# Kernel tuning notes

Measured on AMD Instinct MI355X. Metric: run time of the kernel, lower is better.

## Reference

```python
import jax, jax.numpy as jnp
import numpy as np

B, T, D, A = 4, 4096, 1024, 64
RINGS = 2

def _build_graph_matrix(A, rings):
    # W[a_dst, a_src] = 1/len(neigh) for src in {a_dst-rings..a_dst+rings} within bounds (mean reduce)
    W = np.zeros((A, A), dtype=np.float32)
    for a in range(A):
        neigh = [n for n in range(a - rings, a + rings + 1) if 0 <= n < A]
        W[a, neigh] = 1.0 / len(neigh)
    return jnp.asarray(W)

def setup_inputs() -> dict:
    key = jax.random.key(0)
    k0, k1, k2 = jax.random.split(key, 3)
    x = jax.random.normal(k0, (B, T, D), dtype=jnp.float32)
    # contiguous-ish 1D region assignment of tokens to anchors
    assign = jnp.sort(jax.random.randint(k1, (T,), 0, A)).astype(jnp.int32)
    counts = jnp.clip(jnp.zeros((A,), jnp.float32).at[assign].add(1.0), 1.0, None)
    W_proj = jax.random.normal(k2, (D, D), dtype=jnp.float32) * (1.0 / np.sqrt(D))
    gate = jnp.float32(0.1)
    W_graph = _build_graph_matrix(A, RINGS)
    return {"x": x, "W_proj": W_proj, "gate": gate, "assign": assign,
            "W_graph": W_graph, "counts": counts, "hops": 1}

def reference(x, W_proj, gate, assign, W_graph, counts, hops):
    Bx, Tx, Dx = x.shape
    Ax = counts.shape[0]
    # pool_per_anchor (mean): scatter-add tokens into anchors, divide by counts
    anchor = jnp.zeros((Bx, Ax, Dx), x.dtype).at[:, assign, :].add(x)
    anchor = anchor / counts[None, :, None]
    # neighbor_aggregate: out = einsum('bcd,ac->bad', out, W) per hop
    agg = anchor
    for _ in range(max(1, int(hops))):
        agg = jnp.einsum('ac,bcd->bad', W_graph, agg)
    # broadcast_from_anchor: gather each token's anchor feature
    fb = agg[:, assign, :]  # [B,T,D]
    # residual with gated linear projection (dropout identity in eval)
    return x + (fb @ W_proj.T) * jnp.tanh(gate)
```

## Files before the change

kernel.cpp:

```cpp
#include <hip/hip_runtime.h>
#include <cmath>


typedef __attribute__((ext_vector_type(8))) short bf16x8;
typedef __attribute__((ext_vector_type(4))) float f32x4;

#define OROWS 8

__device__ inline short f2bf(float f) {
    unsigned u = __float_as_uint(f);
    return (short)((u + 0x7FFFu + ((u >> 16) & 1u)) >> 16);
}
__device__ inline int lbound(const int* __restrict__ a, int n, int v) {
    int lo = 0, hi = n;
    while (lo < hi) { int m = (lo + hi) >> 1; if (a[m] < v) lo = m + 1; else hi = m; }
    return lo;
}

__global__ __launch_bounds__(256) void prepanchor_kernel(
        const float* __restrict__ x, const float* __restrict__ counts,
        const int* __restrict__ assign, const float* __restrict__ Wg,
        const int* __restrict__ hops, const float* __restrict__ Wp,
        short* __restrict__ anchorb, short* __restrict__ Wpb, float* __restrict__ M,
        int T, int D, int A, int R) {
    __shared__ float s0[4096];
    __shared__ float s1[4096];
    int bid = blockIdx.x, tid = threadIdx.x;
    int rs = D >> 2;
    if (bid < 2 * R) {
        int u = bid >> 1, half = bid & 1;
        int b = u / A, a = u - (u / A) * A;
        int* sT = (int*)s1;
        if (tid < 2) sT[tid] = lbound(assign, T, a + tid);
        __syncthreads();
        int t0 = sT[0], t1 = sT[1];
        float inv = 1.0f / counts[a];
        int d4 = half * (rs >> 1) + (tid & 127);
        int tp = tid >> 7;
        const float4* x4 = (const float4*)x + (size_t)b * T * rs;
        float4 acc = make_float4(0.f, 0.f, 0.f, 0.f);
        int t = t0 + tp;
        const float4* p = x4 + (size_t)t * rs + d4;
        for (; t + 14 < t1; t += 16) {
            float4 v0 = p[0];
            float4 v1 = p[(size_t)2 * rs];
            float4 v2 = p[(size_t)4 * rs];
            float4 v3 = p[(size_t)6 * rs];
            float4 v4 = p[(size_t)8 * rs];
            float4 v5 = p[(size_t)10 * rs];
            float4 v6 = p[(size_t)12 * rs];
            float4 v7 = p[(size_t)14 * rs];
            acc.x += ((v0.x + v1.x) + (v2.x + v3.x)) + ((v4.x + v5.x) + (v6.x + v7.x));
            acc.y += ((v0.y + v1.y) + (v2.y + v3.y)) + ((v4.y + v5.y) + (v6.y + v7.y));
            acc.z += ((v0.z + v1.z) + (v2.z + v3.z)) + ((v4.z + v5.z) + (v6.z + v7.z));
            acc.w += ((v0.w + v1.w) + (v2.w + v3.w)) + ((v4.w + v5.w) + (v6.w + v7.w));
            p += (size_t)16 * rs;
        }
        for (; t < t1; t += 2) {
            float4 v = *p;
            acc.x += v.x; acc.y += v.y; acc.z += v.z; acc.w += v.w;
            p += (size_t)2 * rs;
        }
        float4* sA = (float4*)s0;
        sA[tid] = acc;
        __syncthreads();
        if (tid < 128) {
            float4 o = sA[tid];
            float4 q = sA[tid + 128];
            o.x = (o.x + q.x) * inv; o.y = (o.y + q.y) * inv;
            o.z = (o.z + q.z) * inv; o.w = (o.w + q.w) * inv;
            short4 ob;
            ob.x = f2bf(o.x); ob.y = f2bf(o.y); ob.z = f2bf(o.z); ob.w = f2bf(o.w);
            ((short4*)anchorb)[(size_t)u * rs + d4] = ob;
        }
    } else if (bid < 2 * R + 256) {
        long long n8 = (long long)D * D / 8;
        for (long long i = (long long)(bid - 2 * R) * 256 + tid; i < n8; i += 256LL * 256LL) {
            const float4* p = (const float4*)Wp + i * 2;
            float4 v0 = p[0], v1 = p[1];
            short4* q = (short4*)Wpb + i * 2;
            short4 o0, o1;
            o0.x = f2bf(v0.x); o0.y = f2bf(v0.y); o0.z = f2bf(v0.z); o0.w = f2bf(v0.w);
            o1.x = f2bf(v1.x); o1.y = f2bf(v1.y); o1.z = f2bf(v1.z); o1.w = f2bf(v1.w);
            q[0] = o0; q[1] = o1;
        }
    } else {
        int n = A * A;
        for (int i = tid; i < n; i += 256) s0[i] = Wg[i];
        int h = hops[0]; if (h < 1) h = 1;
        for (int it = 1; it < h; ++it) {
            __syncthreads();
            for (int i = tid; i < n; i += 256) {
                int r = i / A, c = i - (i / A) * A;
                float s = 0.f;
                for (int k = 0; k < A; ++k) s += Wg[r * A + k] * s0[k * A + c];
                s1[i] = s;
            }
            __syncthreads();
            for (int i = tid; i < n; i += 256) s0[i] = s1[i];
        }
        __syncthreads();
        for (int i = tid; i < n; i += 256) M[i] = s0[i];
    }
}

__global__ __launch_bounds__(256) void ymix_kernel(
        const short* __restrict__ anchorb, const short* __restrict__ Wpb,
        const float* __restrict__ M, float* __restrict__ Y, int D, int A) {
    __shared__ float Z_lds[64][68];
    int b = blockIdx.x, dblk = blockIdx.y;
    int tid = threadIdx.x;
    int wave = tid >> 6, lane = tid & 63;
    int rc = lane & 15, kq = lane >> 4;
    int cpair = wave >> 1, dpair = wave & 1;

    {
        const short* aB0 = anchorb + (size_t)(b * A + cpair * 32 + rc) * D + kq * 8;
        const short* aB1 = aB0 + (size_t)16 * D;
        const short* bB0 = Wpb + (size_t)(dblk * 64 + dpair * 32 + rc) * D + kq * 8;
        const short* bB1 = bB0 + (size_t)16 * D;
        f32x4 acc00 = {0.f,0.f,0.f,0.f}, acc01 = {0.f,0.f,0.f,0.f};
        f32x4 acc10 = {0.f,0.f,0.f,0.f}, acc11 = {0.f,0.f,0.f,0.f};
        for (int k = 0; k < D; k += 32) {
            bf16x8 a0 = *(const bf16x8*)(aB0 + k);
            bf16x8 a1 = *(const bf16x8*)(aB1 + k);
            bf16x8 b0 = *(const bf16x8*)(bB0 + k);
            bf16x8 b1 = *(const bf16x8*)(bB1 + k);
            acc00 = __builtin_amdgcn_mfma_f32_16x16x32_bf16(a0, b0, acc00, 0, 0, 0);
            acc01 = __builtin_amdgcn_mfma_f32_16x16x32_bf16(a0, b1, acc01, 0, 0, 0);
            acc10 = __builtin_amdgcn_mfma_f32_16x16x32_bf16(a1, b0, acc10, 0, 0, 0);
            acc11 = __builtin_amdgcn_mfma_f32_16x16x32_bf16(a1, b1, acc11, 0, 0, 0);
        }
        int zr = cpair * 32 + kq * 4;
        int zc = dpair * 32 + rc;
        #pragma unroll
        for (int j = 0; j < 4; ++j) {
            Z_lds[zr + j][zc]           = acc00[j];
            Z_lds[zr + j][zc + 16]      = acc01[j];
            Z_lds[zr + 16 + j][zc]      = acc10[j];
            Z_lds[zr + 16 + j][zc + 16] = acc11[j];
        }
    }
    __syncthreads();

    for (int i = tid; i < A * 16; i += 256) {
        int a_ = i >> 4, d4 = i & 15;
        const float* Mrow = M + (size_t)a_ * A;
        f32x4 acc = {0.f, 0.f, 0.f, 0.f};
        for (int c = 0; c < 64; ++c) {
            float w = Mrow[c];
            f32x4 z = *(const f32x4*)&Z_lds[c][d4 * 4];
            acc[0] += w * z[0]; acc[1] += w * z[1];
            acc[2] += w * z[2]; acc[3] += w * z[3];
        }
        *(f32x4*)&Y[((size_t)b * A + a_) * D + dblk * 64 + d4 * 4] = acc;
    }
}

__global__ __launch_bounds__(256) void out_kernel(
        const float* __restrict__ x, const float* __restrict__ Y,
        const int* __restrict__ assign, const float* __restrict__ gate,
        float* __restrict__ out, int T, int D, int A) {
    float tg = tanhf(gate[0]);
    int rs = D >> 2;
    int bt0 = blockIdx.x * OROWS;
    const float4* x4 = (const float4*)x;
    const float4* y4 = (const float4*)Y;
    float4* o4 = (float4*)out;
    #pragma unroll
    for (int r = 0; r < OROWS; ++r) {
        int bt = bt0 + r;
        int b = bt / T;
        int t = bt - b * T;
        int a = assign[t];
        const float4* yr = y4 + ((size_t)b * A + a) * rs;
        for (int d4 = threadIdx.x; d4 < rs; d4 += 256) {
            float4 xv = x4[(size_t)bt * rs + d4];
            float4 yv = yr[d4];
            o4[(size_t)bt * rs + d4] = make_float4(xv.x + tg * yv.x, xv.y + tg * yv.y,
                                                   xv.z + tg * yv.z, xv.w + tg * yv.w);
        }
    }
}

extern "C" void kernel_launch(void* const* d_in, const int* in_sizes, int n_in,
                              void* d_out, int out_size, void* d_ws, size_t ws_size,
                              hipStream_t stream) {
    const float* x      = (const float*)d_in[0];
    const float* Wp     = (const float*)d_in[1];
    const float* gate   = (const float*)d_in[2];
    const int*   assign = (const int*)d_in[3];
    const float* Wg     = (const float*)d_in[4];
    const float* counts = (const float*)d_in[5];
    const int*   hops   = (const int*)d_in[6];
    float* out = (float*)d_out;

    int T = in_sizes[3];
    int A = in_sizes[5];
    int D = (int)(sqrt((double)in_sizes[1]) + 0.5);
    int B = (int)(in_sizes[0] / ((long long)T * D));
    int R = B * A;

    float* M       = (float*)d_ws;
    float* Y       = M + (size_t)A * A;
    short* anchorb = (short*)(Y + (size_t)R * D);
    short* Wpb     = anchorb + (size_t)R * D;

    prepanchor_kernel<<<2 * R + 257, 256, 0, stream>>>(x, counts, assign, Wg, hops, Wp,
                                                       anchorb, Wpb, M, T, D, A, R);
    dim3 g(B, D / 64);
    ymix_kernel<<<g, 256, 0, stream>>>(anchorb, Wpb, M, Y, D, A);
    out_kernel<<<B * T / OROWS, 256, 0, stream>>>(x, Y, assign, gate, out, T, D, A);
}
```

Measured before the change: 64.69 us.

## Split anchor pooling into token partials summed inside the MFMA projection

The anchor pooling now splits each anchor's token range into four partial sums written as separate bf16 rows. The ymix GEMM folds the partials in by looping over them along K. The 1/count scaling moves into the graph mixing matrix. This raises pooling-stage parallelism, from 512 to 1024 blocks with a full row each, and drops the LDS reduction, but quadruples the GEMM K work and partial storage. Each partial is also rounded to bf16 separately, which adds rounding error.

Measured after the change: 118.0 us. 1.82x slower.

```diff
diff --git a/kernel.cpp b/kernel.cpp
--- a/kernel.cpp
+++ b/kernel.cpp
@@ -5,6 +5,7 @@
 typedef __attribute__((ext_vector_type(8))) short bf16x8;
 typedef __attribute__((ext_vector_type(4))) float f32x4;
 
+#define SP 4
 #define OROWS 8
 
 __device__ inline short f2bf(float f) {
@@ -17,65 +18,62 @@
     return lo;
 }
 
-__global__ __launch_bounds__(256) void prepanchor_kernel(
+__global__ __launch_bounds__(256) void prep_kernel(
         const float* __restrict__ x, const float* __restrict__ counts,
         const int* __restrict__ assign, const float* __restrict__ Wg,
         const int* __restrict__ hops, const float* __restrict__ Wp,
-        short* __restrict__ anchorb, short* __restrict__ Wpb, float* __restrict__ M,
+        short* __restrict__ partb, short* __restrict__ Wpb, float* __restrict__ Mp,
         int T, int D, int A, int R) {
     __shared__ float s0[4096];
     __shared__ float s1[4096];
     int bid = blockIdx.x, tid = threadIdx.x;
     int rs = D >> 2;
-    if (bid < 2 * R) {
-        int u = bid >> 1, half = bid & 1;
+    int nAB = SP * R;
+    if (bid < nAB) {
+        int part = bid & (SP - 1);
+        int u = bid >> 2;
         int b = u / A, a = u - (u / A) * A;
         int* sT = (int*)s1;
         if (tid < 2) sT[tid] = lbound(assign, T, a + tid);
         __syncthreads();
         int t0 = sT[0], t1 = sT[1];
-        float inv = 1.0f / counts[a];
-        int d4 = half * (rs >> 1) + (tid & 127);
-        int tp = tid >> 7;
+        int len = t1 - t0;
+        int p0 = t0 + (len * part) / SP;
+        int p1 = t0 + (len * (part + 1)) / SP;
         const float4* x4 = (const float4*)x + (size_t)b * T * rs;
-        float4 acc = make_float4(0.f, 0.f, 0.f, 0.f);
-        int t = t0 + tp;
-        const float4* p = x4 + (size_t)t * rs + d4;
-        for (; t + 14 < t1; t += 16) {
-            float4 v0 = p[0];
-            float4 v1 = p[(size_t)2 * rs];
-            float4 v2 = p[(size_t)4 * rs];
-            float4 v3 = p[(size_t)6 * rs];
-            float4 v4 = p[(size_t)8 * rs];
-            float4 v5 = p[(size_t)10 * rs];
-            float4 v6 = p[(size_t)12 * rs];
-            float4 v7 = p[(size_t)14 * rs];
-            acc.x += ((v0.x + v1.x) + (v2.x + v3.x)) + ((v4.x + v5.x) + (v6.x + v7.x));
-            acc.y += ((v0.y + v1.y) + (v2.y + v3.y)) + ((v4.y + v5.y) + (v6.y + v7.y));
-            acc.z += ((v0.z + v1.z) + (v2.z + v3.z)) + ((v4.z + v5.z) + (v6.z + v7.z));
-            acc.w += ((v0.w + v1.w) + (v2.w + v3.w)) + ((v4.w + v5.w) + (v6.w + v7.w));
-            p += (size_t)16 * rs;
-        }
-        for (; t < t1; t += 2) {
-            float4 v = *p;
-            acc.x += v.x; acc.y += v.y; acc.z += v.z; acc.w += v.w;
-            p += (size_t)2 * rs;
-        }
-        float4* sA = (float4*)s0;
-        sA[tid] = acc;
-        __syncthreads();
-        if (tid < 128) {
-            float4 o = sA[tid];
-            float4 q = sA[tid + 128];
-            o.x = (o.x + q.x) * inv; o.y = (o.y + q.y) * inv;
-            o.z = (o.z + q.z) * inv; o.w = (o.w + q.w) * inv;
-            short4 ob;
-            ob.x = f2bf(o.x); ob.y = f2bf(o.y); ob.z = f2bf(o.z); ob.w = f2bf(o.w);
-            ((short4*)anchorb)[(size_t)u * rs + d4] = ob;
-        }
-    } else if (bid < 2 * R + 256) {
+        short4* pb = (short4*)partb + ((size_t)u * SP + part) * rs;
+        for (int d4 = tid; d4 < rs; d4 += 256) {
+            float4 acc = make_float4(0.f, 0.f, 0.f, 0.f);
+            const float4* p = x4 + (size_t)p0 * rs + d4;
+            int t = p0;
+            for (; t + 8 <= p1; t += 8) {
+                float4 v0 = p[0];
+                float4 v1 = p[(size_t)rs];
+                float4 v2 = p[(size_t)2 * rs];
+                float4 v3 = p[(size_t)3 * rs];
+                float4 v4 = p[(size_t)4 * rs];
+                float4 v5 = p[(size_t)5 * rs];
+                float4 v6 = p[(size_t)6 * rs];
+                float4 v7 = p[(size_t)7 * rs];
+                acc.x += ((v0.x + v1.x) + (v2.x + v3.x)) + ((v4.x + v5.x) + (v6.x + v7.x));
+                acc.y += ((v0.y + v1.y) + (v2.y + v3.y)) + ((v4.y + v5.y) + (v6.y + v7.y));
+                acc.z += ((v0.z + v1.z) + (v2.z + v3.z)) + ((v4.z + v5.z) + (v6.z + v7.z));
+                acc.w += ((v0.w + v1.w) + (v2.w + v3.w)) + ((v4.w + v5.w) + (v6.w + v7.w));
+                p += (size_t)8 * rs;
+            }
+            for (; t < p1; ++t) {
+                float4 v = *p;
+                acc.x += v.x; acc.y += v.y; acc.z += v.z; acc.w += v.w;
+                p += rs;
+            }
+            short4 o;
+            o.x = f2bf(acc.x); o.y = f2bf(acc.y);
+            o.z = f2bf(acc.z); o.w = f2bf(acc.w);
+            pb[d4] = o;
+        }
+    } else if (bid < nAB + 256) {
         long long n8 = (long long)D * D / 8;
-        for (long long i = (long long)(bid - 2 * R) * 256 + tid; i < n8; i += 256LL * 256LL) {
+        for (long long i = (long long)(bid - nAB) * 256 + tid; i < n8; i += 256LL * 256LL) {
             const float4* p = (const float4*)Wp + i * 2;
             float4 v0 = p[0], v1 = p[1];
             short4* q = (short4*)Wpb + i * 2;
@@ -100,13 +98,16 @@
             for (int i = tid; i < n; i += 256) s0[i] = s1[i];
         }
         __syncthreads();
-        for (int i = tid; i < n; i += 256) M[i] = s0[i];
+        for (int i = tid; i < n; i += 256) {
+            int c = i - (i / A) * A;
+            Mp[i] = s0[i] / counts[c];
+        }
     }
 }
 
 __global__ __launch_bounds__(256) void ymix_kernel(
-        const short* __restrict__ anchorb, const short* __restrict__ Wpb,
-        const float* __restrict__ M, float* __restrict__ Y, int D, int A) {
+        const short* __restrict__ partb, const short* __restrict__ Wpb,
+        const float* __restrict__ Mp, float* __restrict__ Y, int D, int A) {
     __shared__ float Z_lds[64][68];
     int b = blockIdx.x, dblk = blockIdx.y;
     int tid = threadIdx.x;
@@ -115,21 +116,24 @@
     int cpair = wave >> 1, dpair = wave & 1;
 
     {
-        const short* aB0 = anchorb + (size_t)(b * A + cpair * 32 + rc) * D + kq * 8;
-        const short* aB1 = aB0 + (size_t)16 * D;
         const short* bB0 = Wpb + (size_t)(dblk * 64 + dpair * 32 + rc) * D + kq * 8;
         const short* bB1 = bB0 + (size_t)16 * D;
         f32x4 acc00 = {0.f,0.f,0.f,0.f}, acc01 = {0.f,0.f,0.f,0.f};
         f32x4 acc10 = {0.f,0.f,0.f,0.f}, acc11 = {0.f,0.f,0.f,0.f};
-        for (int k = 0; k < D; k += 32) {
-            bf16x8 a0 = *(const bf16x8*)(aB0 + k);
-            bf16x8 a1 = *(const bf16x8*)(aB1 + k);
-            bf16x8 b0 = *(const bf16x8*)(bB0 + k);
-            bf16x8 b1 = *(const bf16x8*)(bB1 + k);
-            acc00 = __builtin_amdgcn_mfma_f32_16x16x32_bf16(a0, b0, acc00, 0, 0, 0);
-            acc01 = __builtin_amdgcn_mfma_f32_16x16x32_bf16(a0, b1, acc01, 0, 0, 0);
-            acc10 = __builtin_amdgcn_mfma_f32_16x16x32_bf16(a1, b0, acc10, 0, 0, 0);
-            acc11 = __builtin_amdgcn_mfma_f32_16x16x32_bf16(a1, b1, acc11, 0, 0, 0);
+        #pragma unroll
+        for (int p = 0; p < SP; ++p) {
+            const short* aB0 = partb + ((size_t)(b * A + cpair * 32 + rc) * SP + p) * D + kq * 8;
+            const short* aB1 = aB0 + (size_t)16 * SP * D;
+            for (int k = 0; k < D; k += 32) {
+                bf16x8 a0 = *(const bf16x8*)(aB0 + k);
+                bf16x8 a1 = *(const bf16x8*)(aB1 + k);
+                bf16x8 b0 = *(const bf16x8*)(bB0 + k);
+                bf16x8 b1 = *(const bf16x8*)(bB1 + k);
+                acc00 = __builtin_amdgcn_mfma_f32_16x16x32_bf16(a0, b0, acc00, 0, 0, 0);
+                acc01 = __builtin_amdgcn_mfma_f32_16x16x32_bf16(a0, b1, acc01, 0, 0, 0);
+                acc10 = __builtin_amdgcn_mfma_f32_16x16x32_bf16(a1, b0, acc10, 0, 0, 0);
+                acc11 = __builtin_amdgcn_mfma_f32_16x16x32_bf16(a1, b1, acc11, 0, 0, 0);
+            }
         }
         int zr = cpair * 32 + kq * 4;
         int zc = dpair * 32 + rc;
@@ -145,7 +149,7 @@
 
     for (int i = tid; i < A * 16; i += 256) {
         int a_ = i >> 4, d4 = i & 15;
-        const float* Mrow = M + (size_t)a_ * A;
+        const float* Mrow = Mp + (size_t)a_ * A;
         f32x4 acc = {0.f, 0.f, 0.f, 0.f};
         for (int c = 0; c < 64; ++c) {
             float w = Mrow[c];
@@ -201,14 +205,14 @@
     int B = (int)(in_sizes[0] / ((long long)T * D));
     int R = B * A;
 
-    float* M       = (float*)d_ws;
-    float* Y       = M + (size_t)A * A;
-    short* anchorb = (short*)(Y + (size_t)R * D);
-    short* Wpb     = anchorb + (size_t)R * D;
-
-    prepanchor_kernel<<<2 * R + 257, 256, 0, stream>>>(x, counts, assign, Wg, hops, Wp,
-                                                       anchorb, Wpb, M, T, D, A, R);
+    float* Mp    = (float*)d_ws;
+    float* Y     = Mp + (size_t)A * A;
+    short* partb = (short*)(Y + (size_t)R * D);
+    short* Wpb   = partb + (size_t)R * SP * D;
+
+    prep_kernel<<<SP * R + 257, 256, 0, stream>>>(x, counts, assign, Wg, hops, Wp,
+                                                  partb, Wpb, Mp, T, D, A, R);
     dim3 g(B, D / 64);
-    ymix_kernel<<<g, 256, 0, stream>>>(anchorb, Wpb, M, Y, D, A);
+    ymix_kernel<<<g, 256, 0, stream>>>(partb, Wpb, Mp, Y, D, A);
     out_kernel<<<B * T / OROWS, 256, 0, stream>>>(x, Y, assign, gate, out, T, D, A);
 }
```
